# Performance work log

Hardware: AMD Instinct MI355X
Metric: run time of the kernel (lower is better)

Reference implementation:

```python
import jax, jax.numpy as jnp
import numpy as np

HIDDEN = 4096
INTER = 11008
BATCH, SEQ = 2, 2048


def _ternary(key, shape):
    # BitNet b1.58 ternary weights in {-1, 0, +1}
    return jax.random.randint(key, shape, -1, 2).astype(jnp.float32)


def setup_inputs() -> dict:
    key = jax.random.key(0)
    kx, kg, ku, kd = jax.random.split(key, 4)
    x = jax.random.normal(kx, (BATCH, SEQ, HIDDEN), dtype=jnp.float32)
    gate_w = _ternary(kg, (INTER, HIDDEN))
    up_w = _ternary(ku, (INTER, HIDDEN))
    down_w = _ternary(kd, (HIDDEN, INTER))
    # per-tensor absmean scales (dequant factors)
    gate_scale = jnp.float32(0.02)
    up_scale = jnp.float32(0.02)
    down_scale = jnp.float32(0.02)
    return {"x": x, "gate_w": gate_w, "up_w": up_w, "down_w": down_w,
            "gate_scale": gate_scale, "up_scale": up_scale, "down_scale": down_scale}


def reference(x, gate_w, up_w, down_w, gate_scale, up_scale, down_scale):
    # QuantizedLinear: y = (x @ W_q^T) * scale, W_q ternary, bias=False
    gate = jnp.einsum('bsh,ih->bsi', x, gate_w) * gate_scale
    up = jnp.einsum('bsh,ih->bsi', x, up_w) * up_scale
    inter = jax.nn.silu(gate) * up  # SwiGLU
    out = jnp.einsum('bsi,hi->bsh', inter, down_w) * down_scale
    return out
```

## Files before the change

### kernel.cpp

```cpp
#include <hip/hip_runtime.h>


typedef short short8 __attribute__((ext_vector_type(8)));
typedef float f32x4 __attribute__((ext_vector_type(4)));
typedef float fvec4 __attribute__((ext_vector_type(4)));
typedef unsigned short usvec4 __attribute__((ext_vector_type(4)));

#define BM 128
#define BK 32

__device__ __forceinline__ unsigned short f2bf(float f) {
    unsigned int u = __float_as_uint(f);
    u += 0x7FFFu + ((u >> 16) & 1u);
    return (unsigned short)(u >> 16);
}

__global__ void cvt_f32_bf16(const fvec4* __restrict__ src,
                             usvec4* __restrict__ dst, long n4) {
    long i = (long)blockIdx.x * blockDim.x + threadIdx.x;
    if (i < n4) {
        fvec4 v = __builtin_nontemporal_load(src + i);
        usvec4 o;
        o.x = f2bf(v.x); o.y = f2bf(v.y); o.z = f2bf(v.z); o.w = f2bf(v.w);
        dst[i] = o;
    }
}

__global__ void cvt2_f32_bf16(const fvec4* __restrict__ s0,
                              const fvec4* __restrict__ s1,
                              usvec4* __restrict__ d0,
                              usvec4* __restrict__ d1, long n4) {
    long i = (long)blockIdx.x * blockDim.x + threadIdx.x;
    if (i < n4) {
        fvec4 a = __builtin_nontemporal_load(s0 + i);
        fvec4 b = __builtin_nontemporal_load(s1 + i);
        usvec4 oa, ob;
        oa.x = f2bf(a.x); oa.y = f2bf(a.y); oa.z = f2bf(a.z); oa.w = f2bf(a.w);
        ob.x = f2bf(b.x); ob.y = f2bf(b.y); ob.z = f2bf(b.z); ob.w = f2bf(b.w);
        d0[i] = oa;
        d1[i] = ob;
    }
}

#define GLOBAL_TO_LDS(gp, lp)                                                  \
    __builtin_amdgcn_global_load_lds(                                          \
        (__attribute__((address_space(1))) const void*)(gp),                   \
        (__attribute__((address_space(3))) void*)(lp), 16, 0, 0)

__global__ __launch_bounds__(256, 2)
void gemm1_swiglu(const unsigned short* __restrict__ Xb,
                  const unsigned short* __restrict__ Gw,
                  const unsigned short* __restrict__ Uw,
                  unsigned short* __restrict__ inter,
                  const float* __restrict__ gs_p,
                  const float* __restrict__ us_p,
                  int K, int I, int n0) {
    __shared__ unsigned short As[BM * BK];
    __shared__ unsigned short Bg[BM * BK];
    __shared__ unsigned short Bu[BM * BK];

    const int tid = threadIdx.x;
    const int m_base = blockIdx.x * BM;
    const int nb = blockIdx.y * BM;

    f32x4 accg[4][4], accu[4][4];
    const f32x4 z = {0.0f, 0.0f, 0.0f, 0.0f};
#pragma unroll
    for (int i = 0; i < 4; ++i)
#pragma unroll
        for (int j = 0; j < 4; ++j) { accg[i][j] = z; accu[i][j] = z; }

    const int lane = tid & 63;
    const int wid = tid >> 6;
    const int wm = (wid >> 1) * 64;
    const int wn = (wid & 1) * 64;
    const int fr = lane & 15;

    const int c0 = tid, c1 = tid + 256;
    const int r0 = c0 >> 2, r1 = c1 >> 2;
    const int kc0 = (((c0 & 3) ^ ((c0 >> 3) & 3)) << 3);
    const int kc1 = (((c1 & 3) ^ ((c1 >> 3) & 3)) << 3);
    const int ca = (((lane >> 4) ^ ((fr >> 1) & 3)) << 3);

    for (int k0 = 0; k0 < K; k0 += BK) {
        GLOBAL_TO_LDS(Xb + (size_t)(m_base + r0) * K + (k0 + kc0), &As[c0 * 8]);
        GLOBAL_TO_LDS(Xb + (size_t)(m_base + r1) * K + (k0 + kc1), &As[c1 * 8]);
        GLOBAL_TO_LDS(Gw + (size_t)(nb + r0) * K + (k0 + kc0), &Bg[c0 * 8]);
        GLOBAL_TO_LDS(Gw + (size_t)(nb + r1) * K + (k0 + kc1), &Bg[c1 * 8]);
        GLOBAL_TO_LDS(Uw + (size_t)(nb + r0) * K + (k0 + kc0), &Bu[c0 * 8]);
        GLOBAL_TO_LDS(Uw + (size_t)(nb + r1) * K + (k0 + kc1), &Bu[c1 * 8]);
        __syncthreads();

        short8 a[4], bg[4], bu[4];
#pragma unroll
        for (int i = 0; i < 4; ++i) {
            a[i]  = *(const short8*)(&As[(wm + i * 16 + fr) * BK + ca]);
            bg[i] = *(const short8*)(&Bg[(wn + i * 16 + fr) * BK + ca]);
            bu[i] = *(const short8*)(&Bu[(wn + i * 16 + fr) * BK + ca]);
        }
#pragma unroll
        for (int mi = 0; mi < 4; ++mi)
#pragma unroll
            for (int ni = 0; ni < 4; ++ni) {
                accg[mi][ni] = __builtin_amdgcn_mfma_f32_16x16x32_bf16(
                    a[mi], bg[ni], accg[mi][ni], 0, 0, 0);
                accu[mi][ni] = __builtin_amdgcn_mfma_f32_16x16x32_bf16(
                    a[mi], bu[ni], accu[mi][ni], 0, 0, 0);
            }
        __syncthreads();
    }

    const float gsc = *gs_p;
    const float usc = *us_p;
    const int row0 = m_base + wm + (lane >> 4) * 4;
    const int col0 = n0 + nb + wn + fr;
#pragma unroll
    for (int mi = 0; mi < 4; ++mi)
#pragma unroll
        for (int ni = 0; ni < 4; ++ni)
#pragma unroll
            for (int r = 0; r < 4; ++r) {
                float g = accg[mi][ni][r] * gsc;
                float u = accu[mi][ni][r] * usc;
                float s = g / (1.0f + __expf(-g));
                inter[(size_t)(row0 + mi * 16 + r) * I + (col0 + ni * 16)] =
                    f2bf(s * u);
            }
}

__global__ __launch_bounds__(256, 2)
void gemm2_down(const unsigned short* __restrict__ Ab,
                const unsigned short* __restrict__ Dw,
                float* __restrict__ out,
                const float* __restrict__ ds_p,
                int K, int H, int n0) {
    __shared__ unsigned short As[BM * BK];
    __shared__ unsigned short B0[BM * BK];
    __shared__ unsigned short B1[BM * BK];

    const int tid = threadIdx.x;
    const int m_base = blockIdx.x * BM;
    const int nb = blockIdx.y * 256;

    f32x4 acc0[4][4], acc1[4][4];
    const f32x4 z = {0.0f, 0.0f, 0.0f, 0.0f};
#pragma unroll
    for (int i = 0; i < 4; ++i)
#pragma unroll
        for (int j = 0; j < 4; ++j) { acc0[i][j] = z; acc1[i][j] = z; }

    const int lane = tid & 63;
    const int wid = tid >> 6;
    const int wm = (wid >> 1) * 64;
    const int wn = (wid & 1) * 64;
    const int fr = lane & 15;

    const int c0 = tid, c1 = tid + 256;
    const int r0 = c0 >> 2, r1 = c1 >> 2;
    const int kc0 = (((c0 & 3) ^ ((c0 >> 3) & 3)) << 3);
    const int kc1 = (((c1 & 3) ^ ((c1 >> 3) & 3)) << 3);
    const int ca = (((lane >> 4) ^ ((fr >> 1) & 3)) << 3);

    const unsigned short* D0 = Dw + (size_t)nb * K;
    const unsigned short* D1 = Dw + (size_t)(nb + BM) * K;

    for (int k0 = 0; k0 < K; k0 += BK) {
        GLOBAL_TO_LDS(Ab + (size_t)(m_base + r0) * K + (k0 + kc0), &As[c0 * 8]);
        GLOBAL_TO_LDS(Ab + (size_t)(m_base + r1) * K + (k0 + kc1), &As[c1 * 8]);
        GLOBAL_TO_LDS(D0 + (size_t)r0 * K + (k0 + kc0), &B0[c0 * 8]);
        GLOBAL_TO_LDS(D0 + (size_t)r1 * K + (k0 + kc1), &B0[c1 * 8]);
        GLOBAL_TO_LDS(D1 + (size_t)r0 * K + (k0 + kc0), &B1[c0 * 8]);
        GLOBAL_TO_LDS(D1 + (size_t)r1 * K + (k0 + kc1), &B1[c1 * 8]);
        __syncthreads();

        short8 a[4], b0[4], b1[4];
#pragma unroll
        for (int i = 0; i < 4; ++i) {
            a[i]  = *(const short8*)(&As[(wm + i * 16 + fr) * BK + ca]);
            b0[i] = *(const short8*)(&B0[(wn + i * 16 + fr) * BK + ca]);
            b1[i] = *(const short8*)(&B1[(wn + i * 16 + fr) * BK + ca]);
        }
#pragma unroll
        for (int mi = 0; mi < 4; ++mi)
#pragma unroll
            for (int ni = 0; ni < 4; ++ni) {
                acc0[mi][ni] = __builtin_amdgcn_mfma_f32_16x16x32_bf16(
                    a[mi], b0[ni], acc0[mi][ni], 0, 0, 0);
                acc1[mi][ni] = __builtin_amdgcn_mfma_f32_16x16x32_bf16(
                    a[mi], b1[ni], acc1[mi][ni], 0, 0, 0);
            }
        __syncthreads();
    }

    const float dsc = *ds_p;
    const int row0 = m_base + wm + (lane >> 4) * 4;
    const int colA = n0 + nb + wn + fr;
    const int colB = colA + BM;
#pragma unroll
    for (int mi = 0; mi < 4; ++mi)
#pragma unroll
        for (int ni = 0; ni < 4; ++ni)
#pragma unroll
            for (int r = 0; r < 4; ++r) {
                const size_t rowoff = (size_t)(row0 + mi * 16 + r) * H;
                out[rowoff + (colA + ni * 16)] = acc0[mi][ni][r] * dsc;
                out[rowoff + (colB + ni * 16)] = acc1[mi][ni][r] * dsc;
            }
}

extern "C" void kernel_launch(void* const* d_in, const int* in_sizes, int n_in,
                              void* d_out, int out_size, void* d_ws, size_t ws_size,
                              hipStream_t stream) {
    (void)in_sizes; (void)n_in; (void)out_size;
    const float* x  = (const float*)d_in[0];
    const float* gw = (const float*)d_in[1];
    const float* uw = (const float*)d_in[2];
    const float* dw = (const float*)d_in[3];
    const float* gs = (const float*)d_in[4];
    const float* us = (const float*)d_in[5];
    const float* ds = (const float*)d_in[6];
    float* out = (float*)d_out;

    const long M = 4096;
    const long Kh = 4096;
    const long I = 11008;
    const long H = 4096;

    char* ws = (char*)d_ws;
    unsigned short* Xb = (unsigned short*)ws;
    unsigned short* inter = (unsigned short*)(ws + M * Kh * 2);
    const size_t used = (size_t)M * Kh * 2 + (size_t)M * I * 2;
    if (ws_size < used + 2 * (size_t)256 * I * 2) return;
    char* wbuf = ws + used;
    const size_t avail = ws_size - used;

    {
        long n4 = M * Kh / 4;
        cvt_f32_bf16<<<dim3((unsigned)((n4 + 255) / 256)), dim3(256), 0, stream>>>(
            (const fvec4*)x, (usvec4*)Xb, n4);
    }

    long mr1 = (long)(avail / ((size_t)2 * Kh * 2));
    mr1 = (mr1 / 128) * 128;
    if (mr1 > 5504) mr1 = 5504;
    if (mr1 < 128) mr1 = 128;
    unsigned short* Wg = (unsigned short*)wbuf;
    unsigned short* Wu = (unsigned short*)(wbuf + (size_t)mr1 * Kh * 2);
    for (long n0 = 0; n0 < I; n0 += mr1) {
        long rc = (I - n0 < mr1) ? (I - n0) : mr1;
        long e4 = rc * Kh / 4;
        unsigned cb = (unsigned)((e4 + 255) / 256);
        cvt2_f32_bf16<<<dim3(cb), dim3(256), 0, stream>>>(
            (const fvec4*)(gw + n0 * Kh), (const fvec4*)(uw + n0 * Kh),
            (usvec4*)Wg, (usvec4*)Wu, e4);
        gemm1_swiglu<<<dim3((unsigned)(M / BM), (unsigned)(rc / BM)), dim3(256), 0, stream>>>(
            Xb, Wg, Wu, inter, gs, us, (int)Kh, (int)I, (int)n0);
    }

    long mr2 = (long)(avail / ((size_t)I * 2));
    mr2 = (mr2 / 256) * 256;
    if (mr2 > H) mr2 = H;
    if (mr2 < 256) mr2 = 256;
    unsigned short* Wd = (unsigned short*)wbuf;
    for (long h0 = 0; h0 < H; h0 += mr2) {
        long rc = (H - h0 < mr2) ? (H - h0) : mr2;
        long e4 = rc * I / 4;
        unsigned cb = (unsigned)((e4 + 255) / 256);
        cvt_f32_bf16<<<dim3(cb), dim3(256), 0, stream>>>(
            (const fvec4*)(dw + h0 * I), (usvec4*)Wd, e4);
        gemm2_down<<<dim3((unsigned)(M / BM), (unsigned)(rc / 256)), dim3(256), 0, stream>>>(
            inter, Wd, out, ds, (int)I, (int)H, (int)h0);
    }
}
```

Measured before the change: 1.618 ms.

## Rewrite GEMMs as 256x256 tiles with 4-stage LDS pipeline and XCD remap

Both GEMM kernels move to 512-thread blocks computing 256x256 tiles. They use a 4-stage dynamic-LDS ring buffer with asynchronous global-to-LDS prefetch, explicit waitcnt and barriers, and setprio around the MFMA bursts. Gate and up weights are interleaved in 16-row groups during conversion, so one B tile holds both and the SwiGLU epilogue pairs adjacent accumulators. Block indices are remapped to group work per XCD, and the gemm1 chunk cap is lifted so the whole intermediate dimension can be done in one pass. The intent is to hide memory latency and raise data reuse per tile, at the cost of 128KB LDS per block, a large register footprint, and fragile manual scheduling that assumes K is a multiple of 32 and at least four tiles long.

```diff
diff --git a/kernel.cpp b/kernel.cpp
--- a/kernel.cpp
+++ b/kernel.cpp
@@ -5,9 +5,6 @@
 typedef float f32x4 __attribute__((ext_vector_type(4)));
 typedef float fvec4 __attribute__((ext_vector_type(4)));
 typedef unsigned short usvec4 __attribute__((ext_vector_type(4)));
-
-#define BM 128
-#define BK 32
 
 __device__ __forceinline__ unsigned short f2bf(float f) {
     unsigned int u = __float_as_uint(f);
@@ -26,19 +23,21 @@
     }
 }
 
-__global__ void cvt2_f32_bf16(const fvec4* __restrict__ s0,
-                              const fvec4* __restrict__ s1,
-                              usvec4* __restrict__ d0,
-                              usvec4* __restrict__ d1, long n4) {
+__global__ void cvt2_f32_bf16_ilv(const fvec4* __restrict__ s0,
+                                  const fvec4* __restrict__ s1,
+                                  usvec4* __restrict__ d, long n4) {
     long i = (long)blockIdx.x * blockDim.x + threadIdx.x;
     if (i < n4) {
+        long j = i >> 10;
+        long c = i & 1023;
+        long Rg = ((j & ~15L) << 1) | (j & 15);
         fvec4 a = __builtin_nontemporal_load(s0 + i);
         fvec4 b = __builtin_nontemporal_load(s1 + i);
         usvec4 oa, ob;
         oa.x = f2bf(a.x); oa.y = f2bf(a.y); oa.z = f2bf(a.z); oa.w = f2bf(a.w);
         ob.x = f2bf(b.x); ob.y = f2bf(b.y); ob.z = f2bf(b.z); ob.w = f2bf(b.w);
-        d0[i] = oa;
-        d1[i] = ob;
+        d[Rg * 1024 + c] = oa;
+        d[(Rg + 16) * 1024 + c] = ob;
     }
 }
 
@@ -47,165 +46,265 @@
         (__attribute__((address_space(1))) const void*)(gp),                   \
         (__attribute__((address_space(3))) void*)(lp), 16, 0, 0)
 
-__global__ __launch_bounds__(256, 2)
+#define BAR() __builtin_amdgcn_s_barrier()
+#define SCHEDB() __builtin_amdgcn_sched_barrier(0)
+#define LGKM0() do { asm volatile("s_waitcnt lgkmcnt(0)" ::: "memory"); SCHEDB(); } while (0)
+#define VMW(n) asm volatile("s_waitcnt vmcnt(" #n ")" ::: "memory")
+
+__device__ __forceinline__ void remap_block(int gy, int& bx, int& by) {
+    int nwg = gy << 4;
+    int orig = blockIdx.y * 16 + blockIdx.x;
+    int q = nwg >> 3, r = nwg & 7;
+    int xcd = orig & 7, lid = orig >> 3;
+    int wg = (xcd < r ? xcd * (q + 1) : r * (q + 1) + (xcd - r) * q) + lid;
+    bx = wg & 15;
+    by = wg >> 4;
+}
+
+__global__ __launch_bounds__(512, 2)
 void gemm1_swiglu(const unsigned short* __restrict__ Xb,
-                  const unsigned short* __restrict__ Gw,
-                  const unsigned short* __restrict__ Uw,
+                  const unsigned short* __restrict__ Wc,
                   unsigned short* __restrict__ inter,
                   const float* __restrict__ gs_p,
                   const float* __restrict__ us_p,
-                  int K, int I, int n0) {
-    __shared__ unsigned short As[BM * BK];
-    __shared__ unsigned short Bg[BM * BK];
-    __shared__ unsigned short Bu[BM * BK];
-
-    const int tid = threadIdx.x;
-    const int m_base = blockIdx.x * BM;
-    const int nb = blockIdx.y * BM;
-
-    f32x4 accg[4][4], accu[4][4];
+                  int K, int I, int n0, int gy) {
+    extern __shared__ unsigned short lds[];
+
+    int bx, by;
+    remap_block(gy, bx, by);
+
+    const int t = threadIdx.x;
+    const int lane = t & 63;
+    const int wid = t >> 6;
+    const int wm = (wid >> 2) * 128;
+    const int wn = (wid & 3) * 64;
+    const int fr = lane & 15;
+    const int ca = (((lane >> 4) ^ ((fr >> 1) & 3)) << 3);
+
+    const int m_base = bx * 256;
+    const long b_row0 = (long)by * 256;
+
+    const int colsw = (((t & 3) ^ ((t >> 3) & 3)) << 3);
+    const unsigned short* pa0 = Xb + (size_t)(m_base + (t >> 2)) * K + colsw;
+    const unsigned short* pa1 = pa0 + (size_t)128 * K;
+    const unsigned short* pb0 = Wc + (size_t)(b_row0 + (t >> 2)) * K + colsw;
+    const unsigned short* pb1 = pb0 + (size_t)128 * K;
+
+    f32x4 acc[8][4];
     const f32x4 z = {0.0f, 0.0f, 0.0f, 0.0f};
 #pragma unroll
-    for (int i = 0; i < 4; ++i)
-#pragma unroll
-        for (int j = 0; j < 4; ++j) { accg[i][j] = z; accu[i][j] = z; }
-
-    const int lane = tid & 63;
-    const int wid = tid >> 6;
-    const int wm = (wid >> 1) * 64;
-    const int wn = (wid & 1) * 64;
-    const int fr = lane & 15;
-
-    const int c0 = tid, c1 = tid + 256;
-    const int r0 = c0 >> 2, r1 = c1 >> 2;
-    const int kc0 = (((c0 & 3) ^ ((c0 >> 3) & 3)) << 3);
-    const int kc1 = (((c1 & 3) ^ ((c1 >> 3) & 3)) << 3);
-    const int ca = (((lane >> 4) ^ ((fr >> 1) & 3)) << 3);
-
-    for (int k0 = 0; k0 < K; k0 += BK) {
-        GLOBAL_TO_LDS(Xb + (size_t)(m_base + r0) * K + (k0 + kc0), &As[c0 * 8]);
-        GLOBAL_TO_LDS(Xb + (size_t)(m_base + r1) * K + (k0 + kc1), &As[c1 * 8]);
-        GLOBAL_TO_LDS(Gw + (size_t)(nb + r0) * K + (k0 + kc0), &Bg[c0 * 8]);
-        GLOBAL_TO_LDS(Gw + (size_t)(nb + r1) * K + (k0 + kc1), &Bg[c1 * 8]);
-        GLOBAL_TO_LDS(Uw + (size_t)(nb + r0) * K + (k0 + kc0), &Bu[c0 * 8]);
-        GLOBAL_TO_LDS(Uw + (size_t)(nb + r1) * K + (k0 + kc1), &Bu[c1 * 8]);
-        __syncthreads();
-
-        short8 a[4], bg[4], bu[4];
-#pragma unroll
-        for (int i = 0; i < 4; ++i) {
-            a[i]  = *(const short8*)(&As[(wm + i * 16 + fr) * BK + ca]);
-            bg[i] = *(const short8*)(&Bg[(wn + i * 16 + fr) * BK + ca]);
-            bu[i] = *(const short8*)(&Bu[(wn + i * 16 + fr) * BK + ca]);
+    for (int i = 0; i < 8; ++i)
+#pragma unroll
+        for (int j = 0; j < 4; ++j) acc[i][j] = z;
+
+    const int aoff = (wm + fr) * 32 + ca;
+    const int boff = (wn + fr) * 32 + ca;
+    const int Kt = K >> 5;
+
+#pragma unroll
+    for (int s = 0; s < 3; ++s) {
+        unsigned short* Aq = lds + s * 8192;
+        unsigned short* Bq = lds + 32768 + s * 8192;
+        GLOBAL_TO_LDS(pa0, Aq + t * 8);
+        GLOBAL_TO_LDS(pa1, Aq + 4096 + t * 8);
+        GLOBAL_TO_LDS(pb0, Bq + t * 8);
+        GLOBAL_TO_LDS(pb1, Bq + 4096 + t * 8);
+        pa0 += 32; pa1 += 32; pb0 += 32; pb1 += 32;
+    }
+    VMW(8);
+    BAR();
+
+    auto KT = [&](int q, int pq, bool pf) {
+        unsigned short* Aq = lds + q * 8192;
+        unsigned short* Bq = lds + 32768 + q * 8192;
+        unsigned short* Ap = lds + pq * 8192;
+        unsigned short* Bp = lds + 32768 + pq * 8192;
+        short8 af[4], bf[4];
+#pragma unroll
+        for (int i = 0; i < 4; ++i)
+            af[i] = *(const short8*)(Aq + aoff + i * 512);
+#pragma unroll
+        for (int n = 0; n < 4; ++n)
+            bf[n] = *(const short8*)(Bq + boff + n * 512);
+        if (pf) {
+            GLOBAL_TO_LDS(pa0, Ap + t * 8);
+            GLOBAL_TO_LDS(pa1, Ap + 4096 + t * 8);
         }
+        SCHEDB(); BAR(); LGKM0();
+        __builtin_amdgcn_s_setprio(1);
 #pragma unroll
         for (int mi = 0; mi < 4; ++mi)
 #pragma unroll
-            for (int ni = 0; ni < 4; ++ni) {
-                accg[mi][ni] = __builtin_amdgcn_mfma_f32_16x16x32_bf16(
-                    a[mi], bg[ni], accg[mi][ni], 0, 0, 0);
-                accu[mi][ni] = __builtin_amdgcn_mfma_f32_16x16x32_bf16(
-                    a[mi], bu[ni], accu[mi][ni], 0, 0, 0);
-            }
-        __syncthreads();
-    }
+            for (int ni = 0; ni < 4; ++ni)
+                acc[mi][ni] = __builtin_amdgcn_mfma_f32_16x16x32_bf16(
+                    af[mi], bf[ni], acc[mi][ni], 0, 0, 0);
+        __builtin_amdgcn_s_setprio(0);
+        SCHEDB(); BAR();
+#pragma unroll
+        for (int i = 0; i < 4; ++i)
+            af[i] = *(const short8*)(Aq + aoff + (4 + i) * 512);
+        if (pf) {
+            GLOBAL_TO_LDS(pb0, Bp + t * 8);
+            GLOBAL_TO_LDS(pb1, Bp + 4096 + t * 8);
+            pa0 += 32; pa1 += 32; pb0 += 32; pb1 += 32;
+        }
+        SCHEDB(); BAR(); LGKM0();
+        __builtin_amdgcn_s_setprio(1);
+#pragma unroll
+        for (int mi = 0; mi < 4; ++mi)
+#pragma unroll
+            for (int ni = 0; ni < 4; ++ni)
+                acc[4 + mi][ni] = __builtin_amdgcn_mfma_f32_16x16x32_bf16(
+                    af[mi], bf[ni], acc[4 + mi][ni], 0, 0, 0);
+        __builtin_amdgcn_s_setprio(0);
+    };
+
+    int kt = 0;
+    for (; kt < Kt - 3; ++kt) {
+        KT(kt & 3, (kt + 3) & 3, true);
+        VMW(8);
+        BAR();
+    }
+    KT(kt & 3, 0, false); VMW(4); BAR(); ++kt;
+    KT(kt & 3, 0, false); VMW(0); BAR(); ++kt;
+    KT(kt & 3, 0, false);
 
     const float gsc = *gs_p;
     const float usc = *us_p;
-    const int row0 = m_base + wm + (lane >> 4) * 4;
-    const int col0 = n0 + nb + wn + fr;
-#pragma unroll
-    for (int mi = 0; mi < 4; ++mi)
-#pragma unroll
-        for (int ni = 0; ni < 4; ++ni)
+    const int row0 = m_base + wm + ((lane >> 4) << 2);
+    const int col0 = n0 + by * 128 + (wn >> 1) + fr;
+#pragma unroll
+    for (int mi = 0; mi < 8; ++mi)
+#pragma unroll
+        for (int p = 0; p < 2; ++p)
 #pragma unroll
             for (int r = 0; r < 4; ++r) {
-                float g = accg[mi][ni][r] * gsc;
-                float u = accu[mi][ni][r] * usc;
+                float g = acc[mi][2 * p][r] * gsc;
+                float u = acc[mi][2 * p + 1][r] * usc;
                 float s = g / (1.0f + __expf(-g));
-                inter[(size_t)(row0 + mi * 16 + r) * I + (col0 + ni * 16)] =
+                inter[(size_t)(row0 + mi * 16 + r) * I + (col0 + p * 16)] =
                     f2bf(s * u);
             }
 }
 
-__global__ __launch_bounds__(256, 2)
+__global__ __launch_bounds__(512, 2)
 void gemm2_down(const unsigned short* __restrict__ Ab,
                 const unsigned short* __restrict__ Dw,
                 float* __restrict__ out,
                 const float* __restrict__ ds_p,
-                int K, int H, int n0) {
-    __shared__ unsigned short As[BM * BK];
-    __shared__ unsigned short B0[BM * BK];
-    __shared__ unsigned short B1[BM * BK];
-
-    const int tid = threadIdx.x;
-    const int m_base = blockIdx.x * BM;
-    const int nb = blockIdx.y * 256;
-
-    f32x4 acc0[4][4], acc1[4][4];
+                int K, int H, int h0, int gy) {
+    extern __shared__ unsigned short lds[];
+
+    int bx, by;
+    remap_block(gy, bx, by);
+
+    const int t = threadIdx.x;
+    const int lane = t & 63;
+    const int wid = t >> 6;
+    const int wm = (wid >> 2) * 128;
+    const int wn = (wid & 3) * 64;
+    const int fr = lane & 15;
+    const int ca = (((lane >> 4) ^ ((fr >> 1) & 3)) << 3);
+
+    const int m_base = bx * 256;
+    const long b_row0 = (long)by * 256;
+
+    const int colsw = (((t & 3) ^ ((t >> 3) & 3)) << 3);
+    const unsigned short* pa0 = Ab + (size_t)(m_base + (t >> 2)) * K + colsw;
+    const unsigned short* pa1 = pa0 + (size_t)128 * K;
+    const unsigned short* pb0 = Dw + (size_t)(b_row0 + (t >> 2)) * K + colsw;
+    const unsigned short* pb1 = pb0 + (size_t)128 * K;
+
+    f32x4 acc[8][4];
     const f32x4 z = {0.0f, 0.0f, 0.0f, 0.0f};
 #pragma unroll
-    for (int i = 0; i < 4; ++i)
-#pragma unroll
-        for (int j = 0; j < 4; ++j) { acc0[i][j] = z; acc1[i][j] = z; }
-
-    const int lane = tid & 63;
-    const int wid = tid >> 6;
-    const int wm = (wid >> 1) * 64;
-    const int wn = (wid & 1) * 64;
-    const int fr = lane & 15;
-
-    const int c0 = tid, c1 = tid + 256;
-    const int r0 = c0 >> 2, r1 = c1 >> 2;
-    const int kc0 = (((c0 & 3) ^ ((c0 >> 3) & 3)) << 3);
-    const int kc1 = (((c1 & 3) ^ ((c1 >> 3) & 3)) << 3);
-    const int ca = (((lane >> 4) ^ ((fr >> 1) & 3)) << 3);
-
-    const unsigned short* D0 = Dw + (size_t)nb * K;
-    const unsigned short* D1 = Dw + (size_t)(nb + BM) * K;
-
-    for (int k0 = 0; k0 < K; k0 += BK) {
-        GLOBAL_TO_LDS(Ab + (size_t)(m_base + r0) * K + (k0 + kc0), &As[c0 * 8]);
-        GLOBAL_TO_LDS(Ab + (size_t)(m_base + r1) * K + (k0 + kc1), &As[c1 * 8]);
-        GLOBAL_TO_LDS(D0 + (size_t)r0 * K + (k0 + kc0), &B0[c0 * 8]);
-        GLOBAL_TO_LDS(D0 + (size_t)r1 * K + (k0 + kc1), &B0[c1 * 8]);
-        GLOBAL_TO_LDS(D1 + (size_t)r0 * K + (k0 + kc0), &B1[c0 * 8]);
-        GLOBAL_TO_LDS(D1 + (size_t)r1 * K + (k0 + kc1), &B1[c1 * 8]);
-        __syncthreads();
-
-        short8 a[4], b0[4], b1[4];
-#pragma unroll
-        for (int i = 0; i < 4; ++i) {
-            a[i]  = *(const short8*)(&As[(wm + i * 16 + fr) * BK + ca]);
-            b0[i] = *(const short8*)(&B0[(wn + i * 16 + fr) * BK + ca]);
-            b1[i] = *(const short8*)(&B1[(wn + i * 16 + fr) * BK + ca]);
+    for (int i = 0; i < 8; ++i)
+#pragma unroll
+        for (int j = 0; j < 4; ++j) acc[i][j] = z;
+
+    const int aoff = (wm + fr) * 32 + ca;
+    const int boff = (wn + fr) * 32 + ca;
+    const int Kt = K >> 5;
+
+#pragma unroll
+    for (int s = 0; s < 3; ++s) {
+        unsigned short* Aq = lds + s * 8192;
+        unsigned short* Bq = lds + 32768 + s * 8192;
+        GLOBAL_TO_LDS(pa0, Aq + t * 8);
+        GLOBAL_TO_LDS(pa1, Aq + 4096 + t * 8);
+        GLOBAL_TO_LDS(pb0, Bq + t * 8);
+        GLOBAL_TO_LDS(pb1, Bq + 4096 + t * 8);
+        pa0 += 32; pa1 += 32; pb0 += 32; pb1 += 32;
+    }
+    VMW(8);
+    BAR();
+
+    auto KT = [&](int q, int pq, bool pf) {
+        unsigned short* Aq = lds + q * 8192;
+        unsigned short* Bq = lds + 32768 + q * 8192;
+        unsigned short* Ap = lds + pq * 8192;
+        unsigned short* Bp = lds + 32768 + pq * 8192;
+        short8 af[4], bf[4];
+#pragma unroll
+        for (int i = 0; i < 4; ++i)
+            af[i] = *(const short8*)(Aq + aoff + i * 512);
+#pragma unroll
+        for (int n = 0; n < 4; ++n)
+            bf[n] = *(const short8*)(Bq + boff + n * 512);
+        if (pf) {
+            GLOBAL_TO_LDS(pa0, Ap + t * 8);
+            GLOBAL_TO_LDS(pa1, Ap + 4096 + t * 8);
         }
+        SCHEDB(); BAR(); LGKM0();
+        __builtin_amdgcn_s_setprio(1);
 #pragma unroll
         for (int mi = 0; mi < 4; ++mi)
 #pragma unroll
-            for (int ni = 0; ni < 4; ++ni) {
-                acc0[mi][ni] = __builtin_amdgcn_mfma_f32_16x16x32_bf16(
-                    a[mi], b0[ni], acc0[mi][ni], 0, 0, 0);
-                acc1[mi][ni] = __builtin_amdgcn_mfma_f32_16x16x32_bf16(
-                    a[mi], b1[ni], acc1[mi][ni], 0, 0, 0);
-            }
-        __syncthreads();
-    }
+            for (int ni = 0; ni < 4; ++ni)
+                acc[mi][ni] = __builtin_amdgcn_mfma_f32_16x16x32_bf16(
+                    af[mi], bf[ni], acc[mi][ni], 0, 0, 0);
+        __builtin_amdgcn_s_setprio(0);
+        SCHEDB(); BAR();
+#pragma unroll
+        for (int i = 0; i < 4; ++i)
+            af[i] = *(const short8*)(Aq + aoff + (4 + i) * 512);
+        if (pf) {
+            GLOBAL_TO_LDS(pb0, Bp + t * 8);
+            GLOBAL_TO_LDS(pb1, Bp + 4096 + t * 8);
+            pa0 += 32; pa1 += 32; pb0 += 32; pb1 += 32;
+        }
+        SCHEDB(); BAR(); LGKM0();
+        __builtin_amdgcn_s_setprio(1);
+#pragma unroll
+        for (int mi = 0; mi < 4; ++mi)
+#pragma unroll
+            for (int ni = 0; ni < 4; ++ni)
+                acc[4 + mi][ni] = __builtin_amdgcn_mfma_f32_16x16x32_bf16(
+                    af[mi], bf[ni], acc[4 + mi][ni], 0, 0, 0);
+        __builtin_amdgcn_s_setprio(0);
+    };
+
+    int kt = 0;
+    for (; kt < Kt - 3; ++kt) {
+        KT(kt & 3, (kt + 3) & 3, true);
+        VMW(8);
+        BAR();
+    }
+    KT(kt & 3, 0, false); VMW(4); BAR(); ++kt;
+    KT(kt & 3, 0, false); VMW(0); BAR(); ++kt;
+    KT(kt & 3, 0, false);
 
     const float dsc = *ds_p;
-    const int row0 = m_base + wm + (lane >> 4) * 4;
-    const int colA = n0 + nb + wn + fr;
-    const int colB = colA + BM;
-#pragma unroll
-    for (int mi = 0; mi < 4; ++mi)
+    const int row0 = m_base + wm + ((lane >> 4) << 2);
+    const int col0 = h0 + by * 256 + wn + fr;
+#pragma unroll
+    for (int mi = 0; mi < 8; ++mi)
 #pragma unroll
         for (int ni = 0; ni < 4; ++ni)
 #pragma unroll
-            for (int r = 0; r < 4; ++r) {
-                const size_t rowoff = (size_t)(row0 + mi * 16 + r) * H;
-                out[rowoff + (colA + ni * 16)] = acc0[mi][ni][r] * dsc;
-                out[rowoff + (colB + ni * 16)] = acc1[mi][ni][r] * dsc;
-            }
+            for (int r = 0; r < 4; ++r)
+                out[(size_t)(row0 + mi * 16 + r) * H + (col0 + ni * 16)] =
+                    acc[mi][ni][r] * dsc;
 }
 
 extern "C" void kernel_launch(void* const* d_in, const int* in_sizes, int n_in,
@@ -226,6 +325,11 @@
     const long I = 11008;
     const long H = 4096;
 
+    (void)hipFuncSetAttribute(reinterpret_cast<const void*>(gemm1_swiglu),
+                              hipFuncAttributeMaxDynamicSharedMemorySize, 131072);
+    (void)hipFuncSetAttribute(reinterpret_cast<const void*>(gemm2_down),
+                              hipFuncAttributeMaxDynamicSharedMemorySize, 131072);
+
     char* ws = (char*)d_ws;
     unsigned short* Xb = (unsigned short*)ws;
     unsigned short* inter = (unsigned short*)(ws + M * Kh * 2);
@@ -242,19 +346,19 @@
 
     long mr1 = (long)(avail / ((size_t)2 * Kh * 2));
     mr1 = (mr1 / 128) * 128;
-    if (mr1 > 5504) mr1 = 5504;
+    if (mr1 > I) mr1 = I;
     if (mr1 < 128) mr1 = 128;
-    unsigned short* Wg = (unsigned short*)wbuf;
-    unsigned short* Wu = (unsigned short*)(wbuf + (size_t)mr1 * Kh * 2);
+    unsigned short* Wc = (unsigned short*)wbuf;
     for (long n0 = 0; n0 < I; n0 += mr1) {
         long rc = (I - n0 < mr1) ? (I - n0) : mr1;
         long e4 = rc * Kh / 4;
         unsigned cb = (unsigned)((e4 + 255) / 256);
-        cvt2_f32_bf16<<<dim3(cb), dim3(256), 0, stream>>>(
+        cvt2_f32_bf16_ilv<<<dim3(cb), dim3(256), 0, stream>>>(
             (const fvec4*)(gw + n0 * Kh), (const fvec4*)(uw + n0 * Kh),
-            (usvec4*)Wg, (usvec4*)Wu, e4);
-        gemm1_swiglu<<<dim3((unsigned)(M / BM), (unsigned)(rc / BM)), dim3(256), 0, stream>>>(
-            Xb, Wg, Wu, inter, gs, us, (int)Kh, (int)I, (int)n0);
+            (usvec4*)Wc, e4);
+        unsigned gy = (unsigned)(rc / 128);
+        gemm1_swiglu<<<dim3(16, gy), dim3(512), 131072, stream>>>(
+            Xb, Wc, inter, gs, us, (int)Kh, (int)I, (int)n0, (int)gy);
     }
 
     long mr2 = (long)(avail / ((size_t)I * 2));
@@ -268,7 +372,8 @@
         unsigned cb = (unsigned)((e4 + 255) / 256);
         cvt_f32_bf16<<<dim3(cb), dim3(256), 0, stream>>>(
             (const fvec4*)(dw + h0 * I), (usvec4*)Wd, e4);
-        gemm2_down<<<dim3((unsigned)(M / BM), (unsigned)(rc / 256)), dim3(256), 0, stream>>>(
-            inter, Wd, out, ds, (int)I, (int)H, (int)h0);
-    }
-}
+        unsigned gy = (unsigned)(rc / 256);
+        gemm2_down<<<dim3(16, gy), dim3(512), 131072, stream>>>(
+            inter, Wd, out, ds, (int)I, (int)H, (int)h0, (int)gy);
+    }
+}
```

Measured after the change: 1.427 ms. -11.8%, faster.
